# Performance work log

Measured on AMD Instinct MI355X. Metric: run time of the kernel, lower is better.

## Reference

```python
import jax, jax.numpy as jnp
import numpy as np

N = 100000
NLAYERS = 4
NPROP = 2
NGRAPHS = 50


def gcn_conv(x, edge_index, W, b):
    """PyG GCNConv: h = x@W; out[d] = sum_e norm_e * h[src_e] (+ self loops), norm = D^-1/2 A_hat D^-1/2."""
    n = x.shape[0]
    loop = jnp.arange(n, dtype=edge_index.dtype)
    src = jnp.concatenate([edge_index[0], loop])
    dst = jnp.concatenate([edge_index[1], loop])
    deg = jax.ops.segment_sum(jnp.ones(src.shape[0], x.dtype), dst, num_segments=n)
    dinv = jax.lax.rsqrt(deg)  # deg >= 1 thanks to self loops
    norm = (dinv[src] * dinv[dst])[:, None]
    h = x @ W
    return jax.ops.segment_sum(h[src] * norm, dst, num_segments=n) + b


def setup_inputs() -> dict:
    key = jax.random.key(0)
    ks = jax.random.split(key, 16)
    inp = {
        "x": jax.random.normal(ks[0], (N, 16), jnp.float32),
        "feature_mtx_static": jax.random.normal(ks[1], (N, 32), jnp.float32),
        "edge_index": jax.random.randint(ks[2], (2, 400000), 0, N, jnp.int32),
        "inner_edges": jax.random.randint(ks[3], (NLAYERS, 2, 300000), 0, N, jnp.int32),
        "forward_edges": jax.random.randint(ks[4], (NLAYERS, 2, 300000), 0, N, jnp.int32),
        "backward_edges": jax.random.randint(ks[5], (NLAYERS, 2, 300000), 0, N, jnp.int32),
        "layers": jax.random.randint(ks[6], (N,), 0, NLAYERS, jnp.int32),
        "batch": jnp.sort(jax.random.randint(ks[7], (N,), 0, NGRAPHS, jnp.int32)),
        "W_up": jax.random.normal(ks[8], (16, 256), jnp.float32) * 0.25,
        "b_up": jax.random.normal(ks[9], (256,), jnp.float32) * 0.02,
        "W_in": jax.random.normal(ks[10], (288, 256), jnp.float32) * 0.06,
        "b_in": jax.random.normal(ks[11], (256,), jnp.float32) * 0.02,
        "W_fw": jax.random.normal(ks[12], (288, 256), jnp.float32) * 0.06,
        "b_fw": jax.random.normal(ks[13], (256,), jnp.float32) * 0.02,
        "W_lin": jax.random.normal(ks[14], (256, 1), jnp.float32) * 0.06,
        "b_lin": jax.random.normal(ks[15], (1,), jnp.float32) * 0.02,
    }
    return inp


def reference(x, feature_mtx_static, edge_index, inner_edges, forward_edges,
              backward_edges, layers, batch, W_up, b_up, W_in, b_in,
              W_fw, b_fw, W_lin, b_lin):
    def addstatic(h):
        return jnp.concatenate([h, feature_mtx_static], axis=1)

    x = gcn_conv(x, edge_index, W_up, b_up)
    partial_inner = x  # placeholder; overwritten in forward sweep
    for _ in range(NPROP):
        for il in range(NLAYERS):
            layermask = layers == il
            partial_inner = gcn_conv(addstatic(x), inner_edges[il], W_in, b_in)
            x = jnp.where(layermask[:, None], partial_inner, x)
            next_layer_mask = layers == il + 1
            partial_forward = gcn_conv(addstatic(x), forward_edges[il], W_fw, b_fw)
            x = jnp.where(next_layer_mask[:, None], partial_forward, x)
        x = jax.nn.relu(x)
        for il in range(NLAYERS - 1, -1, -1):
            # NOTE: original code computes forward_conv on backward_edges here but
            # assigns from the stale `partial_inner` (dead compute skipped).
            previous_layer_mask = layers == il - 1
            x = jnp.where(previous_layer_mask[:, None], partial_inner, x)
            layermask = layers == il
            partial_backward = gcn_conv(addstatic(x), inner_edges[il], W_in, b_in)
            x = jnp.where(layermask[:, None], partial_backward, x)
        x = jax.nn.relu(x)

    pooled = jax.ops.segment_sum(x, batch, num_segments=NGRAPHS)  # [G, 256]
    return pooled @ W_lin + b_lin  # [G, 1]
```

## Files before the change

kernel.cpp:

```cpp
#include <hip/hip_runtime.h>

#define N_NODES 100000
#define NLAYERS 4
#define NPROP 2
#define NGRAPHS 50
#define NE_MAIN 400000
#define NE_SET 300000
#define NSETS 9
#define CSR_TOTAL (NE_MAIN + 8 * NE_SET)
#define ASTR 296
#define WFSZ (9 * 16 * 512)
#define PCHUNK 4096
#define NCHK 25

typedef __attribute__((ext_vector_type(8))) short bf8_t;
typedef __attribute__((ext_vector_type(4))) float f4_t;

__device__ __align__(16) unsigned short g_x[(size_t)N_NODES * 256];
__device__ __align__(16) unsigned short g_pi[(size_t)N_NODES * 256];
__device__ __align__(16) unsigned short g_fsb[(size_t)N_NODES * 32];
__device__ __align__(16) float g_agg16[(size_t)N_NODES * 16];
__device__ __align__(16) float g_dinv[NSETS * N_NODES];
__device__ __align__(16) float g_pooled[NGRAPHS * 256];
__device__ __align__(16) unsigned short g_Wfh[2 * WFSZ];
__device__ __align__(16) unsigned short g_Wfl[2 * WFSZ];
__device__ int g_deg[NSETS * N_NODES];
__device__ int g_cur[NSETS * N_NODES];
__device__ int g_off[NSETS * (N_NODES + 1)];
__device__ int g_part[NSETS * NCHK];
__device__ __align__(8) int2 g_csr[CSR_TOTAL];
__device__ int g_cnt[4];
__device__ int g_lists[NLAYERS * N_NODES];

__host__ __device__ inline int csr_base(int slot) {
    return slot == 0 ? 0 : NE_MAIN + (slot - 1) * NE_SET;
}

__device__ inline unsigned short f2bf(float f) {
    unsigned u = __float_as_uint(f);
    return (unsigned short)((u + 0x7fffu + ((u >> 16) & 1u)) >> 16);
}
__device__ inline float bf2f(unsigned short b) {
    return __uint_as_float(((unsigned)b) << 16);
}
__device__ inline float4 ldbf4(const unsigned short* p) {
    ushort4 u = *(const ushort4*)p;
    float4 f;
    f.x = bf2f(u.x); f.y = bf2f(u.y); f.z = bf2f(u.z); f.w = bf2f(u.w);
    return f;
}

__device__ inline void edge_decode(int t, const int* ei, const int* inner, const int* fwd,
                                   int& slot, const int*& es, const int*& ed, int& e) {
    if (t < NE_MAIN) {
        slot = 0; e = t; es = ei; ed = ei + NE_MAIN;
    } else {
        int r = t - NE_MAIN;
        int grp = r / NE_SET;
        e = r - grp * NE_SET;
        slot = 1 + grp;
        const int* base = (grp < 4) ? (inner + grp * 2 * NE_SET)
                                    : (fwd + (grp - 4) * 2 * NE_SET);
        es = base; ed = base + NE_SET;
    }
}


__global__ __launch_bounds__(256) void k_init() {
    int i = blockIdx.x * blockDim.x + threadIdx.x;
    if (i < NSETS * N_NODES) g_deg[i] = 0;
    if (i < NGRAPHS * 256) g_pooled[i] = 0.f;
    if (i < 4) g_cnt[i] = 0;
}

__global__ __launch_bounds__(256) void k_fsb(const float* __restrict__ fs) {
    int i = blockIdx.x * blockDim.x + threadIdx.x;
    if (i < N_NODES * 32) g_fsb[i] = f2bf(fs[i]);
}

__global__ __launch_bounds__(256) void k_count_all(const int* __restrict__ ei,
                                                   const int* __restrict__ inner,
                                                   const int* __restrict__ fwd) {
    int t = blockIdx.x * blockDim.x + threadIdx.x;
    if (t >= CSR_TOTAL) return;
    int slot, e; const int *es, *ed;
    edge_decode(t, ei, inner, fwd, slot, es, ed, e);
    atomicAdd(&g_deg[slot * N_NODES + ed[e]], 1);
}

__global__ __launch_bounds__(256) void k_dinv() {
    int i = blockIdx.x * blockDim.x + threadIdx.x;
    if (i < NSETS * N_NODES) g_dinv[i] = rsqrtf(1.0f + (float)g_deg[i]);
}

__global__ __launch_bounds__(256) void k_wt(const float* __restrict__ W, int which) {
    int t = blockIdx.x * blockDim.x + threadIdx.x;
    if (t >= 288 * 256) return;
    int k = t >> 8, n = t & 255;
    int kb = k >> 5, kq = k & 31, quad = kq >> 3, ke = kq & 7;
    int nt = n >> 4, m = n & 15, lane = quad * 16 + m;
    int idx = which * WFSZ + (kb * 16 + nt) * 512 + lane * 8 + ke;
    float w = W[t];
    unsigned short h = f2bf(w);
    unsigned short l = f2bf(w - bf2f(h));
    g_Wfh[idx] = h;
    g_Wfl[idx] = l;
}


__global__ __launch_bounds__(256) void k_scan_a() {
    int b = blockIdx.x;
    int set = b / NCHK, ch = b % NCHK;
    const int* deg = g_deg + (size_t)set * N_NODES;
    int base = ch * PCHUNK + threadIdx.x * 16;
    int s = 0;
#pragma unroll
    for (int j = 0; j < 16; j++) {
        int id = base + j;
        if (id < N_NODES) s += deg[id];
    }
    __shared__ int sm[256];
    sm[threadIdx.x] = s;
    __syncthreads();
    for (int o = 128; o > 0; o >>= 1) {
        if (threadIdx.x < o) sm[threadIdx.x] += sm[threadIdx.x + o];
        __syncthreads();
    }
    if (threadIdx.x == 0) g_part[b] = sm[0];
}

__global__ __launch_bounds__(1024) void k_scan_b() {
    int wv = threadIdx.x >> 6, lane = threadIdx.x & 63;
    if (wv >= NSETS) return;
    int v = (lane < NCHK) ? g_part[wv * NCHK + lane] : 0;
    int orig = v;
    for (int o = 1; o < 32; o <<= 1) {
        int u = __shfl_up(v, o);
        if (lane >= o) v += u;
    }
    if (lane < NCHK) g_part[wv * NCHK + lane] = v - orig;
}

__global__ __launch_bounds__(256) void k_scan_c() {
    int b = blockIdx.x;
    int set = b / NCHK, ch = b % NCHK;
    const int* deg = g_deg + (size_t)set * N_NODES;
    int* off = g_off + (size_t)set * (N_NODES + 1);
    int* cur = g_cur + (size_t)set * N_NODES;
    int t = threadIdx.x;
    int base = ch * PCHUNK + t * 16;
    int v[16];
    int s = 0;
#pragma unroll
    for (int j = 0; j < 16; j++) {
        int id = base + j;
        v[j] = (id < N_NODES) ? deg[id] : 0;
        s += v[j];
    }
    __shared__ int sm[256];
    sm[t] = s;
    __syncthreads();
    for (int o = 1; o < 256; o <<= 1) {
        int u = (t >= o) ? sm[t - o] : 0;
        __syncthreads();
        sm[t] += u;
        __syncthreads();
    }
    int run = g_part[b] + sm[t] - s;
#pragma unroll
    for (int j = 0; j < 16; j++) {
        int id = base + j;
        if (id < N_NODES) { off[id] = run; cur[id] = run; }
        run += v[j];
    }
    if (ch == NCHK - 1 && t == 255) off[N_NODES] = (set == 0) ? NE_MAIN : NE_SET;
}

__global__ __launch_bounds__(256) void k_fill_all(const int* __restrict__ ei,
                                                  const int* __restrict__ inner,
                                                  const int* __restrict__ fwd) {
    int t = blockIdx.x * blockDim.x + threadIdx.x;
    if (t >= CSR_TOTAL) return;
    int slot, e; const int *es, *ed;
    edge_decode(t, ei, inner, fwd, slot, es, ed, e);
    int s = es[e], d = ed[e];
    int pos = atomicAdd(&g_cur[slot * N_NODES + d], 1);
    float nrm = g_dinv[slot * N_NODES + s] * g_dinv[slot * N_NODES + d];
    g_csr[csr_base(slot) + pos] = make_int2(s, __float_as_int(nrm));
}

__global__ __launch_bounds__(256) void k_lists(const int* __restrict__ layers) {
    __shared__ int lcnt[4];
    __shared__ int lbase[4];
    int i = blockIdx.x * blockDim.x + threadIdx.x;
    if (threadIdx.x < 4) lcnt[threadIdx.x] = 0;
    __syncthreads();
    int l = -1, p = 0;
    if (i < N_NODES) {
        l = layers[i];
        p = atomicAdd(&lcnt[l], 1);
    }
    __syncthreads();
    if (threadIdx.x < 4) lbase[threadIdx.x] = atomicAdd(&g_cnt[threadIdx.x], lcnt[threadIdx.x]);
    __syncthreads();
    if (l >= 0) g_lists[l * N_NODES + lbase[l] + p] = i;
}


__global__ __launch_bounds__(256) void k_gather16(const float* __restrict__ xin) {
    int g = blockIdx.x * blockDim.x + threadIdx.x;
    int i = g >> 4, lane = g & 15;
    if (i >= N_NODES) return;
    float dv = g_dinv[i];
    float acc = dv * dv * xin[i * 16 + lane];
    int e0 = g_off[i], e1 = g_off[i + 1];
    for (int e = e0; e < e1; e++) {
        int2 sn = g_csr[e];
        acc += __int_as_float(sn.y) * xin[sn.x * 16 + lane];
    }
    g_agg16[i * 16 + lane] = acc;
}

__global__ __launch_bounds__(256) void k_gemm0(const float* __restrict__ W,
                                               const float* __restrict__ bias) {
    __shared__ float a[128];
    int base = blockIdx.x * 8;
    int t = threadIdx.x;
    if (t < 128) a[t] = g_agg16[base * 16 + t];
    __syncthreads();
    float bb = bias[t];
    for (int r = 0; r < 8; r++) {
        float acc = bb;
#pragma unroll
        for (int k = 0; k < 16; k++) acc += a[r * 16 + k] * W[k * 256 + t];
        g_x[(size_t)(base + r) * 256 + t] = f2bf(acc);
    }
}


__global__ __launch_bounds__(256, 4) void k_conv(int slot, int which,
                                                 const float* __restrict__ bias,
                                                 int layer, int topi) {
    int count = (layer >= 0) ? g_cnt[layer] : N_NODES;
    int base = blockIdx.x * 32;
    if (base >= count) return;
    const unsigned short* Wfh = g_Wfh + (size_t)which * WFSZ;
    const unsigned short* Wfl = g_Wfl + (size_t)which * WFSZ;
    unsigned short* out = topi ? g_pi : g_x;

    __shared__ unsigned short lds_h[32 * ASTR];
    __shared__ unsigned short lds_l[32 * ASTR];
    __shared__ int rows_s[32];
    int t = threadIdx.x;
    if (t < 32) {
        int r = base + t;
        rows_s[t] = (r < count) ? ((layer >= 0) ? g_lists[layer * N_NODES + r] : r) : -1;
    }
    __syncthreads();

    int wv = t >> 6, lane = t & 63;

    const int* offp = g_off + (size_t)slot * (N_NODES + 1);
    int cb = csr_base(slot);
    for (int rr = 0; rr < 8; rr++) {
        int lr = wv * 8 + rr;
        int row = rows_s[lr];
        float4 acc = {0.f, 0.f, 0.f, 0.f};
        float4 accb = {0.f, 0.f, 0.f, 0.f};
        float4 accs = {0.f, 0.f, 0.f, 0.f};
        float4 accsb = {0.f, 0.f, 0.f, 0.f};
        if (row >= 0) {
            float dv = g_dinv[(size_t)slot * N_NODES + row];
            float d2 = dv * dv;
            acc = ldbf4(&g_x[(size_t)row * 256 + lane * 4]);
            acc.x *= d2; acc.y *= d2; acc.z *= d2; acc.w *= d2;
            if (lane < 8) {
                accs = ldbf4(&g_fsb[(size_t)row * 32 + lane * 4]);
                accs.x *= d2; accs.y *= d2; accs.z *= d2; accs.w *= d2;
            }
            int e0 = offp[row] + cb, e1 = offp[row + 1] + cb;
            int e = e0;
            for (; e + 1 < e1; e += 2) {
                int2 sa = g_csr[e];
                int2 sb = g_csr[e + 1];
                float na = __int_as_float(sa.y);
                float nb = __int_as_float(sb.y);
                float4 va = ldbf4(&g_x[(size_t)sa.x * 256 + lane * 4]);
                float4 vb = ldbf4(&g_x[(size_t)sb.x * 256 + lane * 4]);
                acc.x += na * va.x; acc.y += na * va.y;
                acc.z += na * va.z; acc.w += na * va.w;
                accb.x += nb * vb.x; accb.y += nb * vb.y;
                accb.z += nb * vb.z; accb.w += nb * vb.w;
                if (lane < 8) {
                    float4 fa = ldbf4(&g_fsb[(size_t)sa.x * 32 + lane * 4]);
                    float4 fb = ldbf4(&g_fsb[(size_t)sb.x * 32 + lane * 4]);
                    accs.x += na * fa.x; accs.y += na * fa.y;
                    accs.z += na * fa.z; accs.w += na * fa.w;
                    accsb.x += nb * fb.x; accsb.y += nb * fb.y;
                    accsb.z += nb * fb.z; accsb.w += nb * fb.w;
                }
            }
            if (e < e1) {
                int2 sa = g_csr[e];
                float na = __int_as_float(sa.y);
                float4 va = ldbf4(&g_x[(size_t)sa.x * 256 + lane * 4]);
                acc.x += na * va.x; acc.y += na * va.y;
                acc.z += na * va.z; acc.w += na * va.w;
                if (lane < 8) {
                    float4 fa = ldbf4(&g_fsb[(size_t)sa.x * 32 + lane * 4]);
                    accs.x += na * fa.x; accs.y += na * fa.y;
                    accs.z += na * fa.z; accs.w += na * fa.w;
                }
            }
            acc.x += accb.x; acc.y += accb.y; acc.z += accb.z; acc.w += accb.w;
            accs.x += accsb.x; accs.y += accsb.y; accs.z += accsb.z; accs.w += accsb.w;
        }
        ushort4 h, l;
        h.x = f2bf(acc.x); l.x = f2bf(acc.x - bf2f(h.x));
        h.y = f2bf(acc.y); l.y = f2bf(acc.y - bf2f(h.y));
        h.z = f2bf(acc.z); l.z = f2bf(acc.z - bf2f(h.z));
        h.w = f2bf(acc.w); l.w = f2bf(acc.w - bf2f(h.w));
        *(ushort4*)&lds_h[lr * ASTR + lane * 4] = h;
        *(ushort4*)&lds_l[lr * ASTR + lane * 4] = l;
        if (lane < 8) {
            ushort4 hs, ls;
            hs.x = f2bf(accs.x); ls.x = f2bf(accs.x - bf2f(hs.x));
            hs.y = f2bf(accs.y); ls.y = f2bf(accs.y - bf2f(hs.y));
            hs.z = f2bf(accs.z); ls.z = f2bf(accs.z - bf2f(hs.z));
            hs.w = f2bf(accs.w); ls.w = f2bf(accs.w - bf2f(hs.w));
            *(ushort4*)&lds_h[lr * ASTR + 256 + lane * 4] = hs;
            *(ushort4*)&lds_l[lr * ASTR + 256 + lane * 4] = ls;
        }
    }
    __syncthreads();

    int m = lane & 15, quad = lane >> 4;
    int n0 = wv * 64;
    f4_t acc2[2][4];
#pragma unroll
    for (int rt = 0; rt < 2; rt++)
#pragma unroll
        for (int ct = 0; ct < 4; ct++) acc2[rt][ct] = (f4_t){0.f, 0.f, 0.f, 0.f};

    for (int kb = 0; kb < 9; kb++) {
        int k0 = kb * 32;
        bf8_t ah0 = *(const bf8_t*)&lds_h[m * ASTR + k0 + quad * 8];
        bf8_t al0 = *(const bf8_t*)&lds_l[m * ASTR + k0 + quad * 8];
        bf8_t ah1 = *(const bf8_t*)&lds_h[(16 + m) * ASTR + k0 + quad * 8];
        bf8_t al1 = *(const bf8_t*)&lds_l[(16 + m) * ASTR + k0 + quad * 8];
#pragma unroll
        for (int ct = 0; ct < 4; ct++) {
            int nt = wv * 4 + ct;
            const bf8_t bh = *(const bf8_t*)&Wfh[(kb * 16 + nt) * 512 + lane * 8];
            const bf8_t bl = *(const bf8_t*)&Wfl[(kb * 16 + nt) * 512 + lane * 8];
            acc2[0][ct] = __builtin_amdgcn_mfma_f32_16x16x32_bf16(ah0, bh, acc2[0][ct], 0, 0, 0);
            acc2[0][ct] = __builtin_amdgcn_mfma_f32_16x16x32_bf16(al0, bh, acc2[0][ct], 0, 0, 0);
            acc2[0][ct] = __builtin_amdgcn_mfma_f32_16x16x32_bf16(ah0, bl, acc2[0][ct], 0, 0, 0);
            acc2[1][ct] = __builtin_amdgcn_mfma_f32_16x16x32_bf16(ah1, bh, acc2[1][ct], 0, 0, 0);
            acc2[1][ct] = __builtin_amdgcn_mfma_f32_16x16x32_bf16(al1, bh, acc2[1][ct], 0, 0, 0);
            acc2[1][ct] = __builtin_amdgcn_mfma_f32_16x16x32_bf16(ah1, bl, acc2[1][ct], 0, 0, 0);
        }
    }
#pragma unroll
    for (int rt = 0; rt < 2; rt++) {
#pragma unroll
        for (int r = 0; r < 4; r++) {
            int row = rows_s[rt * 16 + quad * 4 + r];
            if (row < 0) continue;
#pragma unroll
            for (int ct = 0; ct < 4; ct++) {
                int n = n0 + ct * 16 + m;
                out[(size_t)row * 256 + n] = f2bf(acc2[rt][ct][r] + bias[n]);
            }
        }
    }
}


__global__ __launch_bounds__(256) void k_copy_rows(int layer) {
    int w = (blockIdx.x * blockDim.x + threadIdx.x) >> 5;
    int lane = threadIdx.x & 31;
    if (w >= g_cnt[layer]) return;
    int i = g_lists[layer * N_NODES + w];
    *(uint4*)(g_x + (size_t)i * 256 + lane * 8) =
        *(const uint4*)(g_pi + (size_t)i * 256 + lane * 8);
}

__global__ __launch_bounds__(256) void k_relu() {
    int i = blockIdx.x * blockDim.x + threadIdx.x;
    if (i >= N_NODES * 32) return;
    ushort4 a = ((ushort4*)g_x)[i * 2];
    ushort4 b = ((ushort4*)g_x)[i * 2 + 1];
    a.x = (a.x & 0x8000) ? 0 : a.x; a.y = (a.y & 0x8000) ? 0 : a.y;
    a.z = (a.z & 0x8000) ? 0 : a.z; a.w = (a.w & 0x8000) ? 0 : a.w;
    b.x = (b.x & 0x8000) ? 0 : b.x; b.y = (b.y & 0x8000) ? 0 : b.y;
    b.z = (b.z & 0x8000) ? 0 : b.z; b.w = (b.w & 0x8000) ? 0 : b.w;
    ((ushort4*)g_x)[i * 2] = a;
    ((ushort4*)g_x)[i * 2 + 1] = b;
}

__global__ __launch_bounds__(256) void k_pool(const int* __restrict__ batch) {
    __shared__ int bs[128];
    int i0 = blockIdx.x * 128;
    if (threadIdx.x < 128) {
        int i = i0 + threadIdx.x;
        bs[threadIdx.x] = (i < N_NODES) ? batch[i] : -1;
    }
    __syncthreads();
    int c = threadIdx.x;
    int lim = min(128, N_NODES - i0);
    float acc = 0.f;
    int cur = bs[0];
    for (int ii = 0; ii < lim; ii++) {
        int g = bs[ii];
        if (g != cur) { atomicAdd(&g_pooled[cur * 256 + c], acc); acc = 0.f; cur = g; }
        acc += fmaxf(bf2f(g_x[(size_t)(i0 + ii) * 256 + c]), 0.f);
    }
    atomicAdd(&g_pooled[cur * 256 + c], acc);
}

__global__ void k_final(const float* __restrict__ W_lin, const float* __restrict__ b_lin,
                        float* __restrict__ out) {
    int g = blockIdx.x;
    int lane = threadIdx.x;
    float4 p = *(const float4*)(g_pooled + g * 256 + lane * 4);
    float4 w = *(const float4*)(W_lin + lane * 4);
    float s = p.x * w.x + p.y * w.y + p.z * w.z + p.w * w.w;
    for (int o = 32; o > 0; o >>= 1) s += __shfl_down(s, o);
    if (lane == 0) out[g] = s + b_lin[0];
}


extern "C" void kernel_launch(void* const* d_in, const int* in_sizes, int n_in,
                              void* d_out, int out_size, void* d_ws, size_t ws_size,
                              hipStream_t stream) {
    const float* xin   = (const float*)d_in[0];
    const float* fs    = (const float*)d_in[1];
    const int* ei      = (const int*)d_in[2];
    const int* inner   = (const int*)d_in[3];
    const int* fwd     = (const int*)d_in[4];
    const int* layers  = (const int*)d_in[6];
    const int* batch   = (const int*)d_in[7];
    const float* W_up  = (const float*)d_in[8];
    const float* b_up  = (const float*)d_in[9];
    const float* W_in  = (const float*)d_in[10];
    const float* b_in  = (const float*)d_in[11];
    const float* W_fw  = (const float*)d_in[12];
    const float* b_fw  = (const float*)d_in[13];
    const float* W_lin = (const float*)d_in[14];
    const float* b_lin = (const float*)d_in[15];
    float* out = (float*)d_out;

    k_init<<<(NSETS * N_NODES + 255) / 256, 256, 0, stream>>>();
    k_fsb<<<(N_NODES * 32 + 255) / 256, 256, 0, stream>>>(fs);
    k_wt<<<(288 * 256 + 255) / 256, 256, 0, stream>>>(W_in, 0);
    k_wt<<<(288 * 256 + 255) / 256, 256, 0, stream>>>(W_fw, 1);
    k_count_all<<<(CSR_TOTAL + 255) / 256, 256, 0, stream>>>(ei, inner, fwd);
    k_dinv<<<(NSETS * N_NODES + 255) / 256, 256, 0, stream>>>();
    k_scan_a<<<NSETS * NCHK, 256, 0, stream>>>();
    k_scan_b<<<1, 1024, 0, stream>>>();
    k_scan_c<<<NSETS * NCHK, 256, 0, stream>>>();
    k_fill_all<<<(CSR_TOTAL + 255) / 256, 256, 0, stream>>>(ei, inner, fwd);
    k_lists<<<(N_NODES + 255) / 256, 256, 0, stream>>>(layers);

    k_gather16<<<(N_NODES * 16 + 255) / 256, 256, 0, stream>>>(xin);
    k_gemm0<<<N_NODES / 8, 256, 0, stream>>>(W_up, b_up);

    auto conv = [&](int slot, int which, const float* bias, int layer, int topi) {
        k_conv<<<(N_NODES + 31) / 32, 256, 0, stream>>>(slot, which, bias, layer, topi);
    };

    for (int p = 0; p < NPROP; p++) {
        for (int il = 0; il < NLAYERS; il++) {
            if (il < NLAYERS - 1) {
                conv(1 + il, 0, b_in, il, 0);
                conv(5 + il, 1, b_fw, il + 1, 0);
            } else {
                conv(1 + il, 0, b_in, -1, 1);
                k_copy_rows<<<12500, 256, 0, stream>>>(3);
            }
        }
        k_relu<<<(N_NODES * 32 + 255) / 256, 256, 0, stream>>>();
        for (int il = NLAYERS - 1; il >= 0; il--) {
            if (il >= 1) k_copy_rows<<<12500, 256, 0, stream>>>(il - 1);
            conv(1 + il, 0, b_in, il, 0);
        }
        if (p < NPROP - 1)
            k_relu<<<(N_NODES * 32 + 255) / 256, 256, 0, stream>>>();
    }

    k_pool<<<(N_NODES + 127) / 128, 256, 0, stream>>>(batch);
    k_final<<<NGRAPHS, 64, 0, stream>>>(W_lin, b_lin, out);
}
```

Baseline: 1.606 ms.

## Shrink CSR to source indices, widen gather loads, fuse layer-3 row copy

The CSR now stores only source indices (4 bytes instead of 8) and recomputes the edge norm from dinv on the fly. The conv gather is reorganised so that 16 lanes handle one row with 16-byte loads, letting each wave process four rows at once instead of one row with 8-byte loads. The full-graph conv at the last layer also writes layer-3 rows straight into g_x, which removes a separate copy-rows kernel. The trade-off is an extra dependent dinv load per edge and more registers per thread for the wider accumulators.

```diff
diff --git a/kernel.cpp b/kernel.cpp
--- a/kernel.cpp
+++ b/kernel.cpp
@@ -14,6 +14,7 @@
 #define NCHK 25
 
 typedef __attribute__((ext_vector_type(8))) short bf8_t;
+typedef __attribute__((ext_vector_type(8))) unsigned short us8_t;
 typedef __attribute__((ext_vector_type(4))) float f4_t;
 
 __device__ __align__(16) unsigned short g_x[(size_t)N_NODES * 256];
@@ -28,7 +29,7 @@
 __device__ int g_cur[NSETS * N_NODES];
 __device__ int g_off[NSETS * (N_NODES + 1)];
 __device__ int g_part[NSETS * NCHK];
-__device__ __align__(8) int2 g_csr[CSR_TOTAL];
+__device__ int g_csrs[CSR_TOTAL];
 __device__ int g_cnt[4];
 __device__ int g_lists[NLAYERS * N_NODES];
 
@@ -42,12 +43,6 @@
 }
 __device__ inline float bf2f(unsigned short b) {
     return __uint_as_float(((unsigned)b) << 16);
-}
-__device__ inline float4 ldbf4(const unsigned short* p) {
-    ushort4 u = *(const ushort4*)p;
-    float4 f;
-    f.x = bf2f(u.x); f.y = bf2f(u.y); f.z = bf2f(u.z); f.w = bf2f(u.w);
-    return f;
 }
 
 __device__ inline void edge_decode(int t, const int* ei, const int* inner, const int* fwd,
@@ -185,8 +180,7 @@
     edge_decode(t, ei, inner, fwd, slot, es, ed, e);
     int s = es[e], d = ed[e];
     int pos = atomicAdd(&g_cur[slot * N_NODES + d], 1);
-    float nrm = g_dinv[slot * N_NODES + s] * g_dinv[slot * N_NODES + d];
-    g_csr[csr_base(slot) + pos] = make_int2(s, __float_as_int(nrm));
+    g_csrs[csr_base(slot) + pos] = s;
 }
 
 __global__ __launch_bounds__(256) void k_lists(const int* __restrict__ layers) {
@@ -215,8 +209,8 @@
     float acc = dv * dv * xin[i * 16 + lane];
     int e0 = g_off[i], e1 = g_off[i + 1];
     for (int e = e0; e < e1; e++) {
-        int2 sn = g_csr[e];
-        acc += __int_as_float(sn.y) * xin[sn.x * 16 + lane];
+        int s = g_csrs[e];
+        acc += g_dinv[s] * dv * xin[s * 16 + lane];
     }
     g_agg16[i * 16 + lane] = acc;
 }
@@ -240,6 +234,7 @@
 
 __global__ __launch_bounds__(256, 4) void k_conv(int slot, int which,
                                                  const float* __restrict__ bias,
+                                                 const int* __restrict__ layersp,
                                                  int layer, int topi) {
     int count = (layer >= 0) ? g_cnt[layer] : N_NODES;
     int base = blockIdx.x * 32;
@@ -259,77 +254,86 @@
     __syncthreads();
 
     int wv = t >> 6, lane = t & 63;
-
+    int grp = lane >> 4, gl = lane & 15;
+
+    const float* dinv_s = g_dinv + (size_t)slot * N_NODES;
     const int* offp = g_off + (size_t)slot * (N_NODES + 1);
     int cb = csr_base(slot);
-    for (int rr = 0; rr < 8; rr++) {
-        int lr = wv * 8 + rr;
+    for (int rr = 0; rr < 2; rr++) {
+        int lr = wv * 8 + grp * 2 + rr;
         int row = rows_s[lr];
-        float4 acc = {0.f, 0.f, 0.f, 0.f};
-        float4 accb = {0.f, 0.f, 0.f, 0.f};
-        float4 accs = {0.f, 0.f, 0.f, 0.f};
-        float4 accsb = {0.f, 0.f, 0.f, 0.f};
+        float acc0[8], acc1[8], accf[8];
+#pragma unroll
+        for (int j = 0; j < 8; j++) { acc0[j] = 0.f; acc1[j] = 0.f; accf[j] = 0.f; }
         if (row >= 0) {
-            float dv = g_dinv[(size_t)slot * N_NODES + row];
-            float d2 = dv * dv;
-            acc = ldbf4(&g_x[(size_t)row * 256 + lane * 4]);
-            acc.x *= d2; acc.y *= d2; acc.z *= d2; acc.w *= d2;
-            if (lane < 8) {
-                accs = ldbf4(&g_fsb[(size_t)row * 32 + lane * 4]);
-                accs.x *= d2; accs.y *= d2; accs.z *= d2; accs.w *= d2;
+            float dvr = dinv_s[row];
+            float d2 = dvr * dvr;
+            us8_t u0 = *(const us8_t*)&g_x[(size_t)row * 256 + gl * 8];
+            us8_t u1 = *(const us8_t*)&g_x[(size_t)row * 256 + 128 + gl * 8];
+#pragma unroll
+            for (int j = 0; j < 8; j++) { acc0[j] = d2 * bf2f(u0[j]); acc1[j] = d2 * bf2f(u1[j]); }
+            if (gl < 4) {
+                us8_t uf = *(const us8_t*)&g_fsb[(size_t)row * 32 + gl * 8];
+#pragma unroll
+                for (int j = 0; j < 8; j++) accf[j] = d2 * bf2f(uf[j]);
             }
-            int e0 = offp[row] + cb, e1 = offp[row + 1] + cb;
+            int e0 = offp[row] + cb, e1e = offp[row + 1] + cb;
             int e = e0;
-            for (; e + 1 < e1; e += 2) {
-                int2 sa = g_csr[e];
-                int2 sb = g_csr[e + 1];
-                float na = __int_as_float(sa.y);
-                float nb = __int_as_float(sb.y);
-                float4 va = ldbf4(&g_x[(size_t)sa.x * 256 + lane * 4]);
-                float4 vb = ldbf4(&g_x[(size_t)sb.x * 256 + lane * 4]);
-                acc.x += na * va.x; acc.y += na * va.y;
-                acc.z += na * va.z; acc.w += na * va.w;
-                accb.x += nb * vb.x; accb.y += nb * vb.y;
-                accb.z += nb * vb.z; accb.w += nb * vb.w;
-                if (lane < 8) {
-                    float4 fa = ldbf4(&g_fsb[(size_t)sa.x * 32 + lane * 4]);
-                    float4 fb = ldbf4(&g_fsb[(size_t)sb.x * 32 + lane * 4]);
-                    accs.x += na * fa.x; accs.y += na * fa.y;
-                    accs.z += na * fa.z; accs.w += na * fa.w;
-                    accsb.x += nb * fb.x; accsb.y += nb * fb.y;
-                    accsb.z += nb * fb.z; accsb.w += nb * fb.w;
+            for (; e + 1 < e1e; e += 2) {
+                int sa = g_csrs[e], sb = g_csrs[e + 1];
+                float na = dinv_s[sa] * dvr;
+                float nb = dinv_s[sb] * dvr;
+                us8_t va0 = *(const us8_t*)&g_x[(size_t)sa * 256 + gl * 8];
+                us8_t va1 = *(const us8_t*)&g_x[(size_t)sa * 256 + 128 + gl * 8];
+                us8_t vb0 = *(const us8_t*)&g_x[(size_t)sb * 256 + gl * 8];
+                us8_t vb1 = *(const us8_t*)&g_x[(size_t)sb * 256 + 128 + gl * 8];
+#pragma unroll
+                for (int j = 0; j < 8; j++) {
+                    acc0[j] += na * bf2f(va0[j]); acc1[j] += na * bf2f(va1[j]);
+                    acc0[j] += nb * bf2f(vb0[j]); acc1[j] += nb * bf2f(vb1[j]);
+                }
+                if (gl < 4) {
+                    us8_t fa = *(const us8_t*)&g_fsb[(size_t)sa * 32 + gl * 8];
+                    us8_t fb = *(const us8_t*)&g_fsb[(size_t)sb * 32 + gl * 8];
+#pragma unroll
+                    for (int j = 0; j < 8; j++)
+                        accf[j] += na * bf2f(fa[j]) + nb * bf2f(fb[j]);
                 }
             }
-            if (e < e1) {
-                int2 sa = g_csr[e];
-                float na = __int_as_float(sa.y);
-                float4 va = ldbf4(&g_x[(size_t)sa.x * 256 + lane * 4]);
-                acc.x += na * va.x; acc.y += na * va.y;
-                acc.z += na * va.z; acc.w += na * va.w;
-                if (lane < 8) {
-                    float4 fa = ldbf4(&g_fsb[(size_t)sa.x * 32 + lane * 4]);
-                    accs.x += na * fa.x; accs.y += na * fa.y;
-                    accs.z += na * fa.z; accs.w += na * fa.w;
+            if (e < e1e) {
+                int sa = g_csrs[e];
+                float na = dinv_s[sa] * dvr;
+                us8_t va0 = *(const us8_t*)&g_x[(size_t)sa * 256 + gl * 8];
+                us8_t va1 = *(const us8_t*)&g_x[(size_t)sa * 256 + 128 + gl * 8];
+#pragma unroll
+                for (int j = 0; j < 8; j++) {
+                    acc0[j] += na * bf2f(va0[j]); acc1[j] += na * bf2f(va1[j]);
+                }
+                if (gl < 4) {
+                    us8_t fa = *(const us8_t*)&g_fsb[(size_t)sa * 32 + gl * 8];
+#pragma unroll
+                    for (int j = 0; j < 8; j++) accf[j] += na * bf2f(fa[j]);
                 }
             }
-            acc.x += accb.x; acc.y += accb.y; acc.z += accb.z; acc.w += accb.w;
-            accs.x += accsb.x; accs.y += accsb.y; accs.z += accsb.z; accs.w += accsb.w;
-        }
-        ushort4 h, l;
-        h.x = f2bf(acc.x); l.x = f2bf(acc.x - bf2f(h.x));
-        h.y = f2bf(acc.y); l.y = f2bf(acc.y - bf2f(h.y));
-        h.z = f2bf(acc.z); l.z = f2bf(acc.z - bf2f(h.z));
-        h.w = f2bf(acc.w); l.w = f2bf(acc.w - bf2f(h.w));
-        *(ushort4*)&lds_h[lr * ASTR + lane * 4] = h;
-        *(ushort4*)&lds_l[lr * ASTR + lane * 4] = l;
-        if (lane < 8) {
-            ushort4 hs, ls;
-            hs.x = f2bf(accs.x); ls.x = f2bf(accs.x - bf2f(hs.x));
-            hs.y = f2bf(accs.y); ls.y = f2bf(accs.y - bf2f(hs.y));
-            hs.z = f2bf(accs.z); ls.z = f2bf(accs.z - bf2f(hs.z));
-            hs.w = f2bf(accs.w); ls.w = f2bf(accs.w - bf2f(hs.w));
-            *(ushort4*)&lds_h[lr * ASTR + 256 + lane * 4] = hs;
-            *(ushort4*)&lds_l[lr * ASTR + 256 + lane * 4] = ls;
+        }
+        us8_t h0, l0, h1, l1;
+#pragma unroll
+        for (int j = 0; j < 8; j++) {
+            h0[j] = f2bf(acc0[j]); l0[j] = f2bf(acc0[j] - bf2f(h0[j]));
+            h1[j] = f2bf(acc1[j]); l1[j] = f2bf(acc1[j] - bf2f(h1[j]));
+        }
+        *(us8_t*)&lds_h[lr * ASTR + gl * 8] = h0;
+        *(us8_t*)&lds_h[lr * ASTR + 128 + gl * 8] = h1;
+        *(us8_t*)&lds_l[lr * ASTR + gl * 8] = l0;
+        *(us8_t*)&lds_l[lr * ASTR + 128 + gl * 8] = l1;
+        if (gl < 4) {
+            us8_t hf, lf;
+#pragma unroll
+            for (int j = 0; j < 8; j++) {
+                hf[j] = f2bf(accf[j]); lf[j] = f2bf(accf[j] - bf2f(hf[j]));
+            }
+            *(us8_t*)&lds_h[lr * ASTR + 256 + gl * 8] = hf;
+            *(us8_t*)&lds_l[lr * ASTR + 256 + gl * 8] = lf;
         }
     }
     __syncthreads();
@@ -367,10 +371,13 @@
         for (int r = 0; r < 4; r++) {
             int row = rows_s[rt * 16 + quad * 4 + r];
             if (row < 0) continue;
+            int dual = topi && (layersp[row] == 3);
 #pragma unroll
             for (int ct = 0; ct < 4; ct++) {
                 int n = n0 + ct * 16 + m;
-                out[(size_t)row * 256 + n] = f2bf(acc2[rt][ct][r] + bias[n]);
+                unsigned short v = f2bf(acc2[rt][ct][r] + bias[n]);
+                out[(size_t)row * 256 + n] = v;
+                if (dual) g_x[(size_t)row * 256 + n] = v;
             }
         }
     }
@@ -467,7 +474,7 @@
     k_gemm0<<<N_NODES / 8, 256, 0, stream>>>(W_up, b_up);
 
     auto conv = [&](int slot, int which, const float* bias, int layer, int topi) {
-        k_conv<<<(N_NODES + 31) / 32, 256, 0, stream>>>(slot, which, bias, layer, topi);
+        k_conv<<<(N_NODES + 31) / 32, 256, 0, stream>>>(slot, which, bias, layers, layer, topi);
     };
 
     for (int p = 0; p < NPROP; p++) {
@@ -477,7 +484,6 @@
                 conv(5 + il, 1, b_fw, il + 1, 0);
             } else {
                 conv(1 + il, 0, b_in, -1, 1);
-                k_copy_rows<<<12500, 256, 0, stream>>>(3);
             }
         }
         k_relu<<<(N_NODES * 32 + 255) / 256, 256, 0, stream>>>();
```

Result: faster. 1.508 ms (-6.1%).
